# Kernel optimization log

Measured on AMD Instinct MI355X. Metric: run time of the kernel, lower is better.

## Reference

```python
import jax, jax.numpy as jnp
import numpy as np

N = 20000
E = 320000
DIN = 256
DH = 64
DOUT = 64
H = 8
NEG_SLOPE = 0.2


def _glorot(key, shape):
    fan_in, fan_out = shape[0], shape[-1]
    lim = jnp.sqrt(6.0 / (fan_in + fan_out))
    return jax.random.uniform(key, shape, jnp.float32, -lim, lim)


def setup_inputs() -> dict:
    key = jax.random.key(0)
    ks = jax.random.split(key, 12)
    x = jax.random.normal(ks[0], (N, DIN), jnp.float32)
    edge_index = jax.random.randint(ks[1], (2, E), 0, N, jnp.int32)
    # layer 1: dim_in -> heads*dim_h
    Wl1 = _glorot(ks[2], (DIN, H * DH));  bl1 = jnp.zeros((H * DH,), jnp.float32)
    Wr1 = _glorot(ks[3], (DIN, H * DH));  br1 = jnp.zeros((H * DH,), jnp.float32)
    att1 = _glorot(ks[4], (H, DH))
    bias1 = jnp.zeros((H * DH,), jnp.float32)
    # layer 2: heads*dim_h -> heads*dim_out
    Wl2 = _glorot(ks[5], (H * DH, H * DOUT)); bl2 = jnp.zeros((H * DOUT,), jnp.float32)
    Wr2 = _glorot(ks[6], (H * DH, H * DOUT)); br2 = jnp.zeros((H * DOUT,), jnp.float32)
    att2 = _glorot(ks[7], (H, DOUT))
    bias2 = jnp.zeros((H * DOUT,), jnp.float32)
    return dict(x=x, edge_index=edge_index, Wl1=Wl1, bl1=bl1, Wr1=Wr1, br1=br1,
                att1=att1, bias1=bias1, Wl2=Wl2, bl2=bl2, Wr2=Wr2, br2=br2,
                att2=att2, bias2=bias2)


def _gatv2(x, src, dst, Wl, bl, Wr, br, att, bias_out, heads, out_ch):
    n = x.shape[0]
    l = (x @ Wl + bl).reshape(n, heads, out_ch)   # source transform
    r = (x @ Wr + br).reshape(n, heads, out_ch)   # target transform
    # per-edge GATv2 score: att . LeakyReLU(l_j + r_i)
    e = jax.nn.leaky_relu(l[src] + r[dst], NEG_SLOPE)      # [E, H, C]
    logits = jnp.einsum('ehc,hc->eh', e, att)              # [E, H]
    # segmented softmax over incoming edges of each destination node
    m = jax.ops.segment_max(logits, dst, num_segments=n)   # [N, H]
    expd = jnp.exp(logits - m[dst])
    denom = jax.ops.segment_sum(expd, dst, num_segments=n)
    alpha = expd / denom[dst]                              # [E, H]
    msg = l[src] * alpha[:, :, None]                       # [E, H, C]
    out = jax.ops.segment_sum(msg, dst, num_segments=n)    # [N, H, C]
    return out.reshape(n, heads * out_ch) + bias_out


def reference(x, edge_index, Wl1, bl1, Wr1, br1, att1, bias1,
              Wl2, bl2, Wr2, br2, att2, bias2):
    n = x.shape[0]
    loops = jnp.arange(n, dtype=edge_index.dtype)
    src = jnp.concatenate([edge_index[0], loops])  # GATv2Conv adds self-loops
    dst = jnp.concatenate([edge_index[1], loops])
    # dropout is identity at inference
    h = _gatv2(x, src, dst, Wl1, bl1, Wr1, br1, att1, bias1, H, DH)
    h = jax.nn.elu(h)
    h = _gatv2(h, src, dst, Wl2, bl2, Wr2, br2, att2, bias2, H, DOUT)
    return h, jax.nn.log_softmax(h, axis=1)
```

## Files before the change

### kernel.cpp

```cpp
#include <hip/hip_runtime.h>
#include <math.h>

#define NN   20000
#define NE   320000
#define ET   (NE + NN)
#define D_IN 256
#define DHID 512
#define NLR  1024
#define MPAD 20096

typedef __attribute__((ext_vector_type(8))) short bf16x8;
typedef __attribute__((ext_vector_type(4))) float f32x4;

typedef __attribute__((address_space(3))) uint       lds_uint;
typedef __attribute__((address_space(1))) const uint gbl_uint;
#define ASYNC16(gp, lp) \
    __builtin_amdgcn_global_load_lds((gbl_uint*)(gp), (lds_uint*)(lp), 16, 0, 0)

__device__ __forceinline__ ushort f2bf(float f) {
    uint u = __float_as_uint(f);
    return (ushort)((u + 0x7fffu + ((u >> 16) & 1u)) >> 16);
}


__global__ __launch_bounds__(256) void init_count(int* count) {
    int i = blockIdx.x * 256 + threadIdx.x;
    if (i < NN) count[i] = 1;
}

__global__ __launch_bounds__(256) void hist_kernel(const int* __restrict__ dstv,
                                                   int* __restrict__ count) {
    int e = blockIdx.x * 256 + threadIdx.x;
    if (e < NE) atomicAdd(&count[dstv[e]], 1);
}

__global__ __launch_bounds__(1024) void scan_kernel(const int* __restrict__ count,
                                                    int* __restrict__ offs,
                                                    int* __restrict__ cursor) {
    __shared__ int sm[1024];
    const int CH = 20;
    int t = threadIdx.x;
    int base = t * CH;
    int local[CH];
    int s = 0;
#pragma unroll
    for (int i = 0; i < CH; i++) {
        int idx = base + i;
        int v = (idx < NN) ? count[idx] : 0;
        local[i] = s;
        s += v;
    }
    sm[t] = s;
    __syncthreads();
    for (int o = 1; o < 1024; o <<= 1) {
        int v = (t >= o) ? sm[t - o] : 0;
        __syncthreads();
        sm[t] += v;
        __syncthreads();
    }
    int pref = (t > 0) ? sm[t - 1] : 0;
#pragma unroll
    for (int i = 0; i < CH; i++) {
        int idx = base + i;
        if (idx < NN) {
            int o_ = pref + local[i];
            offs[idx] = o_;
            cursor[idx] = o_;
        }
    }
    if (t == 1023) offs[NN] = sm[1023];
}

__global__ __launch_bounds__(256) void scatter_kernel(const int* __restrict__ srcv,
                                                      const int* __restrict__ dstv,
                                                      int* __restrict__ cursor,
                                                      int* __restrict__ csr_src) {
    int e = blockIdx.x * 256 + threadIdx.x;
    if (e >= ET) return;
    int s, d;
    if (e < NE) { s = srcv[e]; d = dstv[e]; }
    else        { s = e - NE;  d = s; }
    int pos = atomicAdd(&cursor[d], 1);
    csr_src[pos] = s;
}


__global__ __launch_bounds__(256) void convert_x(const float* __restrict__ x,
                                                 ushort* __restrict__ a) {
    long e = ((long)blockIdx.x * 256 + threadIdx.x) * 4;
    if (e >= (long)MPAD * D_IN) return;
    int row = (int)(e >> 8);
    float4 v = make_float4(0.f, 0.f, 0.f, 0.f);
    if (row < NN) v = *(const float4*)&x[e];
    ushort4 o;
    o.x = f2bf(v.x); o.y = f2bf(v.y); o.z = f2bf(v.z); o.w = f2bf(v.w);
    *(ushort4*)&a[e] = o;
}

__global__ __launch_bounds__(256) void zero_pad2(ushort* __restrict__ a) {
    int t = blockIdx.x * 256 + threadIdx.x;
    if (t < (MPAD - NN) * DHID / 4) {
        ushort4 z = {0, 0, 0, 0};
        *(ushort4*)&a[(long)NN * DHID + (long)t * 4] = z;
    }
}

__global__ __launch_bounds__(256) void transpose_w(const float* __restrict__ Wl,
                                                   const float* __restrict__ Wr,
                                                   ushort* __restrict__ Wt, int K) {
    __shared__ float tile[32][33];
    int k0 = blockIdx.x * 32, n0 = blockIdx.y * 32;
    int tx = threadIdx.x & 31, ty = threadIdx.x >> 5;
    const float* __restrict__ W = (n0 < DHID) ? Wl : Wr;
    int nb = (n0 < DHID) ? n0 : n0 - DHID;
#pragma unroll
    for (int r = ty; r < 32; r += 8)
        tile[r][tx] = W[(long)(k0 + r) * DHID + nb + tx];
    __syncthreads();
#pragma unroll
    for (int r = ty; r < 32; r += 8)
        Wt[(long)(n0 + r) * K + k0 + tx] = f2bf(tile[tx][r]);
}


#define BM 128
#define BN 128
#define BK 64

__global__ __launch_bounds__(256) void gemm_mfma(const ushort* __restrict__ A, int K,
                                                 const ushort* __restrict__ Wt,
                                                 const float* __restrict__ bl,
                                                 const float* __restrict__ br,
                                                 ushort* __restrict__ out) {
    __shared__ ushort As[BM * BK];
    __shared__ ushort Bs[BN * BK];

    int t = threadIdx.x;
    int row0 = blockIdx.x * BM;
    int col0 = blockIdx.y * BN;

    int lane = t & 63, w = t >> 6;
    int wr = w >> 1, wc = w & 1;
    int l16 = lane & 15, lhi = lane >> 4;

    f32x4 acc[4][4];
#pragma unroll
    for (int m = 0; m < 4; m++)
#pragma unroll
        for (int n = 0; n < 4; n++)
            acc[m][n] = (f32x4){0.f, 0.f, 0.f, 0.f};

    for (int k0 = 0; k0 < K; k0 += BK) {
#pragma unroll
        for (int q = 0; q < 4; q++) {
            int chunk = q * 256 + t;
            int row = chunk >> 3;
            int il = (chunk & 7) ^ (row & 7);
            ASYNC16(A  + (long)(row0 + row) * K + k0 + il * 8, (char*)As + chunk * 16);
            ASYNC16(Wt + (long)(col0 + row) * K + k0 + il * 8, (char*)Bs + chunk * 16);
        }
        __syncthreads();
#pragma unroll
        for (int kk = 0; kk < 2; kk++) {
            bf16x8 af[4], bfr[4];
#pragma unroll
            for (int m = 0; m < 4; m++) {
                int rl = wr * 64 + m * 16 + l16;
                int off = rl * 128 + ((kk * 64 + lhi * 16) ^ ((rl & 7) << 4));
                af[m] = *(const bf16x8*)((const char*)As + off);
            }
#pragma unroll
            for (int n = 0; n < 4; n++) {
                int rl = wc * 64 + n * 16 + l16;
                int off = rl * 128 + ((kk * 64 + lhi * 16) ^ ((rl & 7) << 4));
                bfr[n] = *(const bf16x8*)((const char*)Bs + off);
            }
#pragma unroll
            for (int m = 0; m < 4; m++)
#pragma unroll
                for (int n = 0; n < 4; n++)
                    acc[m][n] = __builtin_amdgcn_mfma_f32_16x16x32_bf16(af[m], bfr[n], acc[m][n], 0, 0, 0);
        }
        __syncthreads();
    }

    float bvn[4];
#pragma unroll
    for (int n = 0; n < 4; n++) {
        int col = col0 + wc * 64 + n * 16 + l16;
        bvn[n] = (col < DHID) ? bl[col] : br[col - DHID];
    }
#pragma unroll
    for (int m = 0; m < 4; m++) {
        int rbase = row0 + wr * 64 + m * 16 + lhi * 4;
#pragma unroll
        for (int j = 0; j < 4; j++) {
            int row = rbase + j;
            if (row < NN) {
#pragma unroll
                for (int n = 0; n < 4; n++) {
                    int col = col0 + wc * 64 + n * 16 + l16;
                    out[(long)row * NLR + col] = f2bf(acc[m][n][j] + bvn[n]);
                }
            }
        }
    }
}


#define CVT8(u, f)                                  \
    f[0] = __uint_as_float((u).x << 16);            \
    f[1] = __uint_as_float((u).x & 0xffff0000u);    \
    f[2] = __uint_as_float((u).y << 16);            \
    f[3] = __uint_as_float((u).y & 0xffff0000u);    \
    f[4] = __uint_as_float((u).z << 16);            \
    f[5] = __uint_as_float((u).z & 0xffff0000u);    \
    f[6] = __uint_as_float((u).w << 16);            \
    f[7] = __uint_as_float((u).w & 0xffff0000u);

template <int MODE>
__global__ __launch_bounds__(256) void aggregate_kernel(const ushort* __restrict__ lr,
                                                        const float* __restrict__ att,
                                                        const float* __restrict__ bias,
                                                        const int* __restrict__ csr_src,
                                                        const int* __restrict__ offs,
                                                        ushort* __restrict__ out_bf,
                                                        float* __restrict__ out_f32,
                                                        float* __restrict__ out_lsm) {
    int i = blockIdx.x * 4 + (threadIdx.x >> 6);
    int lane = threadIdx.x & 63;
    int c0 = lane << 3;

    uint4 ur = *(const uint4*)(lr + (long)i * NLR + DHID + c0);
    float rv[8];
    CVT8(ur, rv);
    float a06[8], a04[8];
    float4 at0 = *(const float4*)&att[c0];
    float4 at1 = *(const float4*)&att[c0 + 4];
    const float K06 = 0.6f * 1.44269504f, K04 = 0.4f * 1.44269504f;
    a06[0] = at0.x * K06; a06[1] = at0.y * K06; a06[2] = at0.z * K06; a06[3] = at0.w * K06;
    a06[4] = at1.x * K06; a06[5] = at1.y * K06; a06[6] = at1.z * K06; a06[7] = at1.w * K06;
    a04[0] = at0.x * K04; a04[1] = at0.y * K04; a04[2] = at0.z * K04; a04[3] = at0.w * K04;
    a04[4] = at1.x * K04; a04[5] = at1.y * K04; a04[6] = at1.z * K04; a04[7] = at1.w * K04;

    int beg = offs[i], end = offs[i + 1];
    float m = -3.0e38f, d = 0.f;
    float acc[8] = {0.f, 0.f, 0.f, 0.f, 0.f, 0.f, 0.f, 0.f};

    int j = csr_src[beg];
    uint4 v = *(const uint4*)(lr + (long)j * NLR + c0);

    for (int k = beg; k < end; k++) {
        uint4 vc = v;
        int jn = csr_src[k + 1];
        v = *(const uint4*)(lr + (long)jn * NLR + c0);

        float lx[8];
        CVT8(vc, lx);
        float s = 0.f;
#pragma unroll
        for (int c = 0; c < 8; c++) {
            float tt = lx[c] + rv[c];
            s = fmaf(a06[c], tt, s);
            s = fmaf(a04[c], __builtin_fabsf(tt), s);
        }
        s += __shfl_xor(s, 1);
        s += __shfl_xor(s, 2);
        s += __shfl_xor(s, 4);

        float delta = s - m;
        if (__builtin_expect(delta > 8.f, 0)) {
            float sc = exp2f(-delta);
            d *= sc;
#pragma unroll
            for (int c = 0; c < 8; c++) acc[c] *= sc;
            m = s;
            delta = 0.f;
        }
        float wgt = exp2f(delta);
        d += wgt;
#pragma unroll
        for (int c = 0; c < 8; c++) acc[c] = fmaf(wgt, lx[c], acc[c]);
    }

    float inv = 1.f / d;
    float o[8];
    float4 bi0 = *(const float4*)&bias[c0];
    float4 bi1 = *(const float4*)&bias[c0 + 4];
    o[0] = fmaf(acc[0], inv, bi0.x); o[1] = fmaf(acc[1], inv, bi0.y);
    o[2] = fmaf(acc[2], inv, bi0.z); o[3] = fmaf(acc[3], inv, bi0.w);
    o[4] = fmaf(acc[4], inv, bi1.x); o[5] = fmaf(acc[5], inv, bi1.y);
    o[6] = fmaf(acc[6], inv, bi1.z); o[7] = fmaf(acc[7], inv, bi1.w);

    if (MODE == 0) {
#pragma unroll
        for (int c = 0; c < 8; c++) o[c] = (o[c] > 0.f) ? o[c] : expm1f(o[c]);
        uint4 p;
        p.x = (uint)f2bf(o[0]) | ((uint)f2bf(o[1]) << 16);
        p.y = (uint)f2bf(o[2]) | ((uint)f2bf(o[3]) << 16);
        p.z = (uint)f2bf(o[4]) | ((uint)f2bf(o[5]) << 16);
        p.w = (uint)f2bf(o[6]) | ((uint)f2bf(o[7]) << 16);
        *(uint4*)(out_bf + (long)i * DHID + c0) = p;
    } else {
        *(float4*)&out_f32[(long)i * DHID + c0]     = *(float4*)&o[0];
        *(float4*)&out_f32[(long)i * DHID + c0 + 4] = *(float4*)&o[4];
        float mx = o[0];
#pragma unroll
        for (int c = 1; c < 8; c++) mx = fmaxf(mx, o[c]);
#pragma unroll
        for (int off = 1; off < 64; off <<= 1) mx = fmaxf(mx, __shfl_xor(mx, off));
        float se = 0.f;
#pragma unroll
        for (int c = 0; c < 8; c++) se += __expf(o[c] - mx);
#pragma unroll
        for (int off = 1; off < 64; off <<= 1) se += __shfl_xor(se, off);
        float lg = mx + logf(se);
        float l0[8];
#pragma unroll
        for (int c = 0; c < 8; c++) l0[c] = o[c] - lg;
        *(float4*)&out_lsm[(long)i * DHID + c0]     = *(float4*)&l0[0];
        *(float4*)&out_lsm[(long)i * DHID + c0 + 4] = *(float4*)&l0[4];
    }
}


extern "C" void kernel_launch(void* const* d_in, const int* in_sizes, int n_in,
                              void* d_out, int out_size, void* d_ws, size_t ws_size,
                              hipStream_t stream) {
    const float* x     = (const float*)d_in[0];
    const int*   ei    = (const int*)d_in[1];
    const float* Wl1   = (const float*)d_in[2];
    const float* bl1   = (const float*)d_in[3];
    const float* Wr1   = (const float*)d_in[4];
    const float* br1   = (const float*)d_in[5];
    const float* att1  = (const float*)d_in[6];
    const float* bias1 = (const float*)d_in[7];
    const float* Wl2   = (const float*)d_in[8];
    const float* bl2   = (const float*)d_in[9];
    const float* Wr2   = (const float*)d_in[10];
    const float* br2   = (const float*)d_in[11];
    const float* att2  = (const float*)d_in[12];
    const float* bias2 = (const float*)d_in[13];

    float* out = (float*)d_out;
    float* h2  = out;
    float* lsm = out + (long)NN * DHID;

    ushort* lrbuf  = (ushort*)d_ws;
    ushort* Abf    = lrbuf + (long)NN * NLR;
    ushort* Wt1    = Abf + (long)MPAD * DHID;
    ushort* Wt2    = Wt1 + (long)NLR * D_IN;
    int*    csr_src = (int*)(Wt2 + (long)NLR * DHID);
    int*    count   = csr_src + ET;
    int*    offs    = count + NN;
    int*    cursor  = offs + NN + 1;

    const int* srcv = ei;
    const int* dstv = ei + NE;

    convert_x<<<(MPAD * D_IN / 4 + 255) / 256, 256, 0, stream>>>(x, Abf);
    zero_pad2<<<((MPAD - NN) * DHID / 4 + 255) / 256, 256, 0, stream>>>(Abf);
    transpose_w<<<dim3(D_IN / 32, NLR / 32), 256, 0, stream>>>(Wl1, Wr1, Wt1, D_IN);
    transpose_w<<<dim3(DHID / 32, NLR / 32), 256, 0, stream>>>(Wl2, Wr2, Wt2, DHID);

    init_count<<<(NN + 255) / 256, 256, 0, stream>>>(count);
    hist_kernel<<<(NE + 255) / 256, 256, 0, stream>>>(dstv, count);
    scan_kernel<<<1, 1024, 0, stream>>>(count, offs, cursor);
    scatter_kernel<<<(ET + 255) / 256, 256, 0, stream>>>(srcv, dstv, cursor, csr_src);

    dim3 ggrid((NN + BM - 1) / BM, NLR / BN);

    gemm_mfma<<<ggrid, 256, 0, stream>>>(Abf, D_IN, Wt1, bl1, br1, lrbuf);
    aggregate_kernel<0><<<NN / 4, 256, 0, stream>>>(lrbuf, att1, bias1, csr_src, offs, Abf, nullptr, nullptr);

    gemm_mfma<<<ggrid, 256, 0, stream>>>(Abf, DHID, Wt2, bl2, br2, lrbuf);
    aggregate_kernel<1><<<NN / 4, 256, 0, stream>>>(lrbuf, att2, bias2, csr_src, offs, nullptr, h2, lsm);
}
```

Measured before the change: 262.8 us.

## Process destination nodes in degree-descending order for load balance in aggregation

Builds a degree-sorted permutation of nodes with a counting sort (histogram, reverse scan, scatter), and the aggregation kernels use it to map waves to nodes so high-degree nodes run first and each block gets similar degrees. It also clamps the next-edge prefetch index, pads csr_src, and switches the online softmax to rescale on every new maximum instead of only when the jump exceeds a threshold. This adds three small kernel launches and scatters output writes in exchange for less wave imbalance and tail effects.

Result: slower. 370.4 us (+40.9%).

```diff
diff --git a/kernel.cpp b/kernel.cpp
--- a/kernel.cpp
+++ b/kernel.cpp
@@ -4,6 +4,7 @@
 #define NN   20000
 #define NE   320000
 #define ET   (NE + NN)
+#define CPAD 16
 #define D_IN 256
 #define DHID 512
 #define NLR  1024
@@ -23,9 +24,11 @@
 }
 
 
-__global__ __launch_bounds__(256) void init_count(int* count) {
+__global__ __launch_bounds__(256) void init_count(int* count, int* csr_src, int* dhist) {
     int i = blockIdx.x * 256 + threadIdx.x;
     if (i < NN) count[i] = 1;
+    if (i < CPAD) csr_src[ET + i] = 0;
+    if (i < 256) dhist[i] = 0;
 }
 
 __global__ __launch_bounds__(256) void hist_kernel(const int* __restrict__ dstv,
@@ -69,6 +72,33 @@
         }
     }
     if (t == 1023) offs[NN] = sm[1023];
+}
+
+__global__ __launch_bounds__(256) void deg_hist(const int* __restrict__ count,
+                                                int* __restrict__ dhist) {
+    int i = blockIdx.x * 256 + threadIdx.x;
+    if (i < NN) atomicAdd(&dhist[min(count[i], 255)], 1);
+}
+
+__global__ __launch_bounds__(256) void deg_scan(const int* __restrict__ dhist,
+                                                int* __restrict__ dcur) {
+    __shared__ int sm[256];
+    int t = threadIdx.x;
+    sm[t] = dhist[t];
+    __syncthreads();
+    int s = 0;
+    for (int b = t + 1; b < 256; b++) s += sm[b];
+    dcur[t] = s;
+}
+
+__global__ __launch_bounds__(256) void deg_scatter(const int* __restrict__ count,
+                                                   int* __restrict__ dcur,
+                                                   int* __restrict__ perm) {
+    int i = blockIdx.x * 256 + threadIdx.x;
+    if (i < NN) {
+        int pos = atomicAdd(&dcur[min(count[i], 255)], 1);
+        perm[pos] = i;
+    }
 }
 
 __global__ __launch_bounds__(256) void scatter_kernel(const int* __restrict__ srcv,
@@ -224,10 +254,11 @@
                                                         const float* __restrict__ bias,
                                                         const int* __restrict__ csr_src,
                                                         const int* __restrict__ offs,
+                                                        const int* __restrict__ perm,
                                                         ushort* __restrict__ out_bf,
                                                         float* __restrict__ out_f32,
                                                         float* __restrict__ out_lsm) {
-    int i = blockIdx.x * 4 + (threadIdx.x >> 6);
+    int i = perm[blockIdx.x * 4 + (threadIdx.x >> 6)];
     int lane = threadIdx.x & 63;
     int c0 = lane << 3;
 
@@ -252,7 +283,8 @@
 
     for (int k = beg; k < end; k++) {
         uint4 vc = v;
-        int jn = csr_src[k + 1];
+        int kn = (k + 1 < end) ? k + 1 : k;
+        int jn = csr_src[kn];
         v = *(const uint4*)(lr + (long)jn * NLR + c0);
 
         float lx[8];
@@ -268,16 +300,14 @@
         s += __shfl_xor(s, 2);
         s += __shfl_xor(s, 4);
 
-        float delta = s - m;
-        if (__builtin_expect(delta > 8.f, 0)) {
-            float sc = exp2f(-delta);
+        if (s > m) {
+            float sc = exp2f(m - s);
             d *= sc;
 #pragma unroll
             for (int c = 0; c < 8; c++) acc[c] *= sc;
             m = s;
-            delta = 0.f;
-        }
-        float wgt = exp2f(delta);
+        }
+        float wgt = exp2f(s - m);
         d += wgt;
 #pragma unroll
         for (int c = 0; c < 8; c++) acc[c] = fmaf(wgt, lx[c], acc[c]);
@@ -351,9 +381,12 @@
     ushort* Wt1    = Abf + (long)MPAD * DHID;
     ushort* Wt2    = Wt1 + (long)NLR * D_IN;
     int*    csr_src = (int*)(Wt2 + (long)NLR * DHID);
-    int*    count   = csr_src + ET;
+    int*    count   = csr_src + ET + CPAD;
     int*    offs    = count + NN;
     int*    cursor  = offs + NN + 1;
+    int*    perm    = cursor + NN;
+    int*    dhist   = perm + NN;
+    int*    dcur    = dhist + 256;
 
     const int* srcv = ei;
     const int* dstv = ei + NE;
@@ -363,16 +396,19 @@
     transpose_w<<<dim3(D_IN / 32, NLR / 32), 256, 0, stream>>>(Wl1, Wr1, Wt1, D_IN);
     transpose_w<<<dim3(DHID / 32, NLR / 32), 256, 0, stream>>>(Wl2, Wr2, Wt2, DHID);
 
-    init_count<<<(NN + 255) / 256, 256, 0, stream>>>(count);
+    init_count<<<(NN + 255) / 256, 256, 0, stream>>>(count, csr_src, dhist);
     hist_kernel<<<(NE + 255) / 256, 256, 0, stream>>>(dstv, count);
     scan_kernel<<<1, 1024, 0, stream>>>(count, offs, cursor);
+    deg_hist<<<(NN + 255) / 256, 256, 0, stream>>>(count, dhist);
+    deg_scan<<<1, 256, 0, stream>>>(dhist, dcur);
+    deg_scatter<<<(NN + 255) / 256, 256, 0, stream>>>(count, dcur, perm);
     scatter_kernel<<<(ET + 255) / 256, 256, 0, stream>>>(srcv, dstv, cursor, csr_src);
 
     dim3 ggrid((NN + BM - 1) / BM, NLR / BN);
 
     gemm_mfma<<<ggrid, 256, 0, stream>>>(Abf, D_IN, Wt1, bl1, br1, lrbuf);
-    aggregate_kernel<0><<<NN / 4, 256, 0, stream>>>(lrbuf, att1, bias1, csr_src, offs, Abf, nullptr, nullptr);
+    aggregate_kernel<0><<<NN / 4, 256, 0, stream>>>(lrbuf, att1, bias1, csr_src, offs, perm, Abf, nullptr, nullptr);
 
     gemm_mfma<<<ggrid, 256, 0, stream>>>(Abf, DHID, Wt2, bl2, br2, lrbuf);
-    aggregate_kernel<1><<<NN / 4, 256, 0, stream>>>(lrbuf, att2, bias2, csr_src, offs, nullptr, h2, lsm);
-}
+    aggregate_kernel<1><<<NN / 4, 256, 0, stream>>>(lrbuf, att2, bias2, csr_src, offs, perm, nullptr, h2, lsm);
+}
```
